# Optimization experiments

Hardware: AMD Instinct MI355X
Metric: run time of the kernel (lower is better)

## Reference

```python
import jax, jax.numpy as jnp
import numpy as np

K = 8  # num_neighbors
EPS = 1e-12

def _l2_normalize(x):
    n = jnp.sqrt(jnp.sum(x * x, axis=1, keepdims=True))
    return x / jnp.maximum(n, EPS)

def setup_inputs() -> dict:
    key = jax.random.key(0)
    k1, k2, k3, k4 = jax.random.split(key, 4)
    feats = jax.random.normal(k1, (1024, 2048), dtype=jnp.float32)
    bank_features = jax.random.normal(k2, (2048, 2048), dtype=jnp.float32)
    logits = jax.random.normal(k3, (2048, 1000), dtype=jnp.float32)
    bank_probs = jax.nn.softmax(logits, axis=1)  # bank stores softmaxed probs
    image_bank = jax.random.normal(k4, (2048, 3, 224, 224), dtype=jnp.float32)
    return {"feats": feats, "bank_features": bank_features,
            "bank_probs": bank_probs, "image_bank": image_bank}

def reference(feats, bank_features, bank_probs, image_bank):
    # cosine distances: [N, Q]
    dist = 1.0 - _l2_normalize(feats) @ _l2_normalize(bank_features).T
    # original code: topk(largest=True) on distances -> keep faithful
    _, idxs = jax.lax.top_k(dist, K)            # idxs: [N, K]
    grads = jnp.mean(bank_features[idxs], axis=1)   # [N, D]
    pred_probs = jnp.mean(bank_probs[idxs], axis=1)  # [N, C]
    # mean over K neighbor images; loop over small fixed K to avoid a
    # [N, K, 3, 224, 224] (~5 GB) intermediate (torch avoids it by chunking N)
    acc = image_bank[idxs[:, 0]]
    for k in range(1, K):
        acc = acc + image_bank[idxs[:, k]]
    pred_images = acc / K                            # [N, 3, 224, 224]
    pred_labels = jnp.argmax(pred_probs, axis=1)     # [N]
    return pred_labels, pred_probs, pred_images, grads
```

## Files before the change

kernel.cpp:

```cpp
#include <hip/hip_runtime.h>
#include <math.h>

#define NF   1024
#define NB   2048
#define DIM  2048
#define NC   1000
#define IMG  150528
#define IMG4 37632
#define KSEL 8

typedef float f32x4 __attribute__((ext_vector_type(4)));
typedef float f32x2 __attribute__((ext_vector_type(2)));

__global__ __launch_bounds__(256) void norms_kernel(
    const float* __restrict__ feats, const float* __restrict__ bank,
    float* __restrict__ invf, float* __restrict__ invb)
{
    int row = blockIdx.x;
    const float* src;
    float* dst;
    if (row < NF) { src = feats + (size_t)row * DIM; dst = invf + row; }
    else          { src = bank  + (size_t)(row - NF) * DIM; dst = invb + (row - NF); }

    float s = 0.f;
    for (int c = threadIdx.x; c < DIM / 4; c += 256) {
        float4 v = ((const float4*)src)[c];
        s += v.x * v.x + v.y * v.y + v.z * v.z + v.w * v.w;
    }
    __shared__ float red[4];
    for (int off = 32; off; off >>= 1) s += __shfl_down(s, off, 64);
    if ((threadIdx.x & 63) == 0) red[threadIdx.x >> 6] = s;
    __syncthreads();
    if (threadIdx.x == 0) {
        float t = red[0] + red[1] + red[2] + red[3];
        float n = fmaxf(sqrtf(t), 1e-12f);
        *dst = 1.0f / n;
    }
}

#define GBM 128
#define GBN 64
#define GBK 16
#define NCB (NB / GBN)

__global__ __launch_bounds__(256) void dist_kernel(
    const float* __restrict__ A, const float* __restrict__ B,
    const float* __restrict__ invf, const float* __restrict__ invb,
    float* __restrict__ candv, int* __restrict__ candi)
{
    __shared__ float As[2][GBK][GBM];
    __shared__ float Bs[2][GBK][GBN];
    __shared__ float ep[GBM][GBN + 1];

    const int tid  = threadIdx.x;
    const int brow = blockIdx.y * GBM;
    const int bcol = blockIdx.x * GBN;
    const int ty   = tid >> 4;
    const int tx   = tid & 15;

    const int lrow = tid >> 2;
    const int lk   = (tid & 3) * 4;

    f32x2 acc01[8] = {};
    f32x2 acc23[8] = {};

    {
        float4 a0 = *(const float4*)(A + (size_t)(brow + lrow)      * DIM + lk);
        float4 a1 = *(const float4*)(A + (size_t)(brow + lrow + 64) * DIM + lk);
        float4 b0 = *(const float4*)(B + (size_t)(bcol + lrow)      * DIM + lk);
        As[0][lk + 0][lrow] = a0.x; As[0][lk + 1][lrow] = a0.y;
        As[0][lk + 2][lrow] = a0.z; As[0][lk + 3][lrow] = a0.w;
        As[0][lk + 0][lrow + 64] = a1.x; As[0][lk + 1][lrow + 64] = a1.y;
        As[0][lk + 2][lrow + 64] = a1.z; As[0][lk + 3][lrow + 64] = a1.w;
        Bs[0][lk + 0][lrow] = b0.x; Bs[0][lk + 1][lrow] = b0.y;
        Bs[0][lk + 2][lrow] = b0.z; Bs[0][lk + 3][lrow] = b0.w;
    }
    __syncthreads();

    int cur = 0;
    for (int k0 = 0; k0 < DIM; k0 += GBK) {
        const bool has_next = (k0 + GBK) < DIM;
        float4 na0, na1, nb0;
        if (has_next) {
            na0 = *(const float4*)(A + (size_t)(brow + lrow)      * DIM + k0 + GBK + lk);
            na1 = *(const float4*)(A + (size_t)(brow + lrow + 64) * DIM + k0 + GBK + lk);
            nb0 = *(const float4*)(B + (size_t)(bcol + lrow)      * DIM + k0 + GBK + lk);
        }

        #pragma unroll
        for (int k = 0; k < GBK; ++k) {
            float4 av0 = *(const float4*)&As[cur][k][ty * 8];
            float4 av1 = *(const float4*)&As[cur][k][ty * 8 + 4];
            float4 bv  = *(const float4*)&Bs[cur][k][tx * 4];
            f32x2 b01 = {bv.x, bv.y};
            f32x2 b23 = {bv.z, bv.w};
            float a[8] = {av0.x, av0.y, av0.z, av0.w, av1.x, av1.y, av1.z, av1.w};
            #pragma unroll
            for (int i = 0; i < 8; ++i) {
                f32x2 ai = {a[i], a[i]};
                acc01[i] = __builtin_elementwise_fma(ai, b01, acc01[i]);
                acc23[i] = __builtin_elementwise_fma(ai, b23, acc23[i]);
            }
        }

        if (has_next) {
            const int nxt = cur ^ 1;
            As[nxt][lk + 0][lrow] = na0.x; As[nxt][lk + 1][lrow] = na0.y;
            As[nxt][lk + 2][lrow] = na0.z; As[nxt][lk + 3][lrow] = na0.w;
            As[nxt][lk + 0][lrow + 64] = na1.x; As[nxt][lk + 1][lrow + 64] = na1.y;
            As[nxt][lk + 2][lrow + 64] = na1.z; As[nxt][lk + 3][lrow + 64] = na1.w;
            Bs[nxt][lk + 0][lrow] = nb0.x; Bs[nxt][lk + 1][lrow] = nb0.y;
            Bs[nxt][lk + 2][lrow] = nb0.z; Bs[nxt][lk + 3][lrow] = nb0.w;
        }
        __syncthreads();
        cur ^= 1;
    }

    float fi[8], fb[4];
    #pragma unroll
    for (int i = 0; i < 8; ++i) fi[i] = invf[brow + ty * 8 + i];
    #pragma unroll
    for (int j = 0; j < 4; ++j) fb[j] = invb[bcol + tx * 4 + j];
    #pragma unroll
    for (int i = 0; i < 8; ++i) {
        ep[ty * 8 + i][tx * 4 + 0] = 1.0f - acc01[i].x * fi[i] * fb[0];
        ep[ty * 8 + i][tx * 4 + 1] = 1.0f - acc01[i].y * fi[i] * fb[1];
        ep[ty * 8 + i][tx * 4 + 2] = 1.0f - acc23[i].x * fi[i] * fb[2];
        ep[ty * 8 + i][tx * 4 + 3] = 1.0f - acc23[i].y * fi[i] * fb[3];
    }
    __syncthreads();

    if (tid < GBM) {
        float lv[KSEL];
        int   li[KSEL];
        #pragma unroll
        for (int s = 0; s < KSEL; ++s) { lv[s] = -1e30f; li[s] = NB; }
        for (int c = 0; c < GBN; ++c) {
            float v = ep[tid][c];
            if (v > lv[KSEL - 1]) {
                lv[KSEL - 1] = v; li[KSEL - 1] = bcol + c;
                #pragma unroll
                for (int p = KSEL - 1; p > 0; --p) {
                    if (lv[p] > lv[p - 1]) {
                        float tv = lv[p]; lv[p] = lv[p - 1]; lv[p - 1] = tv;
                        int   ti = li[p]; li[p] = li[p - 1]; li[p - 1] = ti;
                    }
                }
            }
        }
        size_t base = ((size_t)(brow + tid) * NCB + blockIdx.x) * KSEL;
        #pragma unroll
        for (int s = 0; s < KSEL; ++s) {
            candv[base + s] = lv[s];
            candi[base + s] = li[s];
        }
    }
}

__global__ __launch_bounds__(256) void final_topk_kernel(
    const float* __restrict__ candv, const int* __restrict__ candi,
    int* __restrict__ idxs)
{
    const int row = blockIdx.x;
    const int t = threadIdx.x;
    __shared__ float cv[256];
    __shared__ int   ci[256];
    __shared__ float rv[256];
    __shared__ int   ri[256];
    cv[t] = candv[(size_t)row * 256 + t];
    ci[t] = candi[(size_t)row * 256 + t];
    __syncthreads();

    for (int sel = 0; sel < KSEL; ++sel) {
        rv[t] = cv[t]; ri[t] = ci[t];
        __syncthreads();
        for (int s = 128; s; s >>= 1) {
            if (t < s) {
                float ov = rv[t + s]; int oi = ri[t + s];
                if (ov > rv[t] || (ov == rv[t] && oi < ri[t])) {
                    rv[t] = ov; ri[t] = oi;
                }
            }
            __syncthreads();
        }
        if (t == 0) idxs[row * KSEL + sel] = ri[0];
        if (cv[t] == rv[0] && ci[t] == ri[0]) cv[t] = -1e30f;
        __syncthreads();
    }
}

#define ITILES 294
#define RPB    4
#define NIMGB  (ITILES * (NF / 8))

__global__ __launch_bounds__(256) void gather_kernel(
    const float* __restrict__ bank_probs, const float* __restrict__ bank_feats,
    const float* __restrict__ image_bank, const int* __restrict__ idxs,
    float* __restrict__ out_labels, float* __restrict__ out_probs,
    float* __restrict__ out_grads,  float* __restrict__ out_images)
{
    const int gid = blockIdx.x;
    const int t = threadIdx.x;
    __shared__ int   id[KSEL];
    __shared__ float rv[256];
    __shared__ int   ri[256];

    if (gid < NF) {
        const int row = gid;
        if (t < KSEL) id[t] = idxs[row * KSEL + t];
        __syncthreads();
        float bv = -1e30f; int bc = NC;
        for (int c = t; c < NC; c += 256) {
            float s = 0.f;
            #pragma unroll
            for (int k = 0; k < KSEL; ++k) s += bank_probs[(size_t)id[k] * NC + c];
            s *= (1.0f / KSEL);
            out_probs[(size_t)row * NC + c] = s;
            if (s > bv) { bv = s; bc = c; }
        }
        rv[t] = bv; ri[t] = bc;
        __syncthreads();
        for (int s = 128; s; s >>= 1) {
            if (t < s) {
                float ov = rv[t + s]; int oi = ri[t + s];
                if (ov > rv[t] || (ov == rv[t] && oi < ri[t])) {
                    rv[t] = ov; ri[t] = oi;
                }
            }
            __syncthreads();
        }
        if (t == 0) out_labels[row] = (float)ri[0];
    } else if (gid < 2 * NF) {
        const int row = gid - NF;
        if (t < KSEL) id[t] = idxs[row * KSEL + t];
        __syncthreads();
        for (int c = t; c < DIM / 4; c += 256) {
            f32x4 acc = {0.f, 0.f, 0.f, 0.f};
            #pragma unroll
            for (int k = 0; k < KSEL; ++k)
                acc += ((const f32x4*)(bank_feats + (size_t)id[k] * DIM))[c];
            ((f32x4*)(out_grads + (size_t)row * DIM))[c] = acc * 0.125f;
        }
    } else {
        const int b = gid - 2 * NF;
        int tile, rowblk;
        if (b < 36864) {
            const int group  = b >> 10;
            const int within = b & 1023;
            rowblk = within >> 3;
            tile   = group * 8 + (within & 7);
        } else {
            const int bb = b - 36864;
            tile   = 288 + bb % 6;
            rowblk = bb / 6;
        }
        const int half = t >> 7;
        const int lane = t & 127;
        const int row0 = rowblk * 8 + half * RPB;
        const int base4 = tile * 128 + lane;

        const int* __restrict__ ip = idxs + row0 * KSEL;
        const f32x4* __restrict__ bank4 = (const f32x4*)image_bank;

        f32x4 v[RPB][KSEL];
        #pragma unroll
        for (int r = 0; r < RPB; ++r)
            #pragma unroll
            for (int k = 0; k < KSEL; ++k)
                v[r][k] = bank4[(size_t)ip[r * KSEL + k] * IMG4 + base4];
        __builtin_amdgcn_sched_barrier(0);

        #pragma unroll
        for (int r = 0; r < RPB; ++r) {
            f32x4 s01 = v[r][0] + v[r][1];
            f32x4 s23 = v[r][2] + v[r][3];
            f32x4 s45 = v[r][4] + v[r][5];
            f32x4 s67 = v[r][6] + v[r][7];
            f32x4 o = ((s01 + s23) + (s45 + s67)) * 0.125f;
            f32x4* outp = (f32x4*)(out_images + (size_t)(row0 + r) * IMG) + base4;
            __builtin_nontemporal_store(o, outp);
        }
    }
}

extern "C" void kernel_launch(void* const* d_in, const int* in_sizes, int n_in,
                              void* d_out, int out_size, void* d_ws, size_t ws_size,
                              hipStream_t stream)
{
    const float* feats      = (const float*)d_in[0];
    const float* bank_feats = (const float*)d_in[1];
    const float* bank_probs = (const float*)d_in[2];
    const float* image_bank = (const float*)d_in[3];

    float* out = (float*)d_out;
    float* out_labels = out;
    float* out_probs  = out + NF;
    float* out_images = out + NF + (size_t)NF * NC;
    float* out_grads  = out + NF + (size_t)NF * NC + (size_t)NF * IMG;

    float* invf  = (float*)d_ws;
    float* invb  = invf + NF;
    int*   idxs  = (int*)(invb + NB);
    float* candv = (float*)(idxs + NF * KSEL);
    int*   candi = (int*)(candv + (size_t)NF * NCB * KSEL);

    norms_kernel<<<NF + NB, 256, 0, stream>>>(feats, bank_feats, invf, invb);

    dim3 ggrid(NCB, NF / GBM);
    dist_kernel<<<ggrid, 256, 0, stream>>>(feats, bank_feats, invf, invb, candv, candi);

    final_topk_kernel<<<NF, 256, 0, stream>>>(candv, candi, idxs);

    gather_kernel<<<2 * NF + NIMGB, 256, 0, stream>>>(
        bank_probs, bank_feats, image_bank, idxs,
        out_labels, out_probs, out_grads, out_images);
}
```

Measured before the change: 646.9 us.

## Remap distance GEMM to 512 threads with 16x1 per-thread micro-tiles

The cosine-distance GEMM block grows from 256 to 512 threads. Each thread now computes a 16-row by 1-column strip: the A values are broadcast per wavefront and each lane takes one B column, instead of the previous 8x4 register tile built on packed f32x2 FMAs. This cuts register pressure per thread and removes LDS bank conflicts on B reads. In exchange, each FMA needs more LDS reads, the packed FMA path is lost, and the top-k selection stage still uses only 128 of the 512 threads.

```diff
diff --git a/kernel.cpp b/kernel.cpp
--- a/kernel.cpp
+++ b/kernel.cpp
@@ -10,7 +10,6 @@
 #define KSEL 8
 
 typedef float f32x4 __attribute__((ext_vector_type(4)));
-typedef float f32x2 __attribute__((ext_vector_type(2)));
 
 __global__ __launch_bounds__(256) void norms_kernel(
     const float* __restrict__ feats, const float* __restrict__ bank,
@@ -43,7 +42,7 @@
 #define GBK 16
 #define NCB (NB / GBN)
 
-__global__ __launch_bounds__(256) void dist_kernel(
+__global__ __launch_bounds__(512) void dist_kernel(
     const float* __restrict__ A, const float* __restrict__ B,
     const float* __restrict__ invf, const float* __restrict__ invb,
     float* __restrict__ candv, int* __restrict__ candi)
@@ -55,78 +54,81 @@
     const int tid  = threadIdx.x;
     const int brow = blockIdx.y * GBM;
     const int bcol = blockIdx.x * GBN;
-    const int ty   = tid >> 4;
-    const int tx   = tid & 15;
-
-    const int lrow = tid >> 2;
-    const int lk   = (tid & 3) * 4;
-
-    f32x2 acc01[8] = {};
-    f32x2 acc23[8] = {};
+    const int r0   = (tid >> 6) * 16;
+    const int lane = tid & 63;
+
+    const int lrowA = tid >> 2;
+    const int lkA   = (tid & 3) * 4;
+
+    float acc[16] = {};
 
     {
-        float4 a0 = *(const float4*)(A + (size_t)(brow + lrow)      * DIM + lk);
-        float4 a1 = *(const float4*)(A + (size_t)(brow + lrow + 64) * DIM + lk);
-        float4 b0 = *(const float4*)(B + (size_t)(bcol + lrow)      * DIM + lk);
-        As[0][lk + 0][lrow] = a0.x; As[0][lk + 1][lrow] = a0.y;
-        As[0][lk + 2][lrow] = a0.z; As[0][lk + 3][lrow] = a0.w;
-        As[0][lk + 0][lrow + 64] = a1.x; As[0][lk + 1][lrow + 64] = a1.y;
-        As[0][lk + 2][lrow + 64] = a1.z; As[0][lk + 3][lrow + 64] = a1.w;
-        Bs[0][lk + 0][lrow] = b0.x; Bs[0][lk + 1][lrow] = b0.y;
-        Bs[0][lk + 2][lrow] = b0.z; Bs[0][lk + 3][lrow] = b0.w;
+        float4 a0 = *(const float4*)(A + (size_t)(brow + lrowA) * DIM + lkA);
+        As[0][lkA + 0][lrowA] = a0.x; As[0][lkA + 1][lrowA] = a0.y;
+        As[0][lkA + 2][lrowA] = a0.z; As[0][lkA + 3][lrowA] = a0.w;
+        if (tid < 256) {
+            float4 b0 = *(const float4*)(B + (size_t)(bcol + lrowA) * DIM + lkA);
+            Bs[0][lkA + 0][lrowA] = b0.x; Bs[0][lkA + 1][lrowA] = b0.y;
+            Bs[0][lkA + 2][lrowA] = b0.z; Bs[0][lkA + 3][lrowA] = b0.w;
+        }
     }
     __syncthreads();
 
     int cur = 0;
     for (int k0 = 0; k0 < DIM; k0 += GBK) {
         const bool has_next = (k0 + GBK) < DIM;
-        float4 na0, na1, nb0;
+        float4 na, nb;
         if (has_next) {
-            na0 = *(const float4*)(A + (size_t)(brow + lrow)      * DIM + k0 + GBK + lk);
-            na1 = *(const float4*)(A + (size_t)(brow + lrow + 64) * DIM + k0 + GBK + lk);
-            nb0 = *(const float4*)(B + (size_t)(bcol + lrow)      * DIM + k0 + GBK + lk);
+            na = *(const float4*)(A + (size_t)(brow + lrowA) * DIM + k0 + GBK + lkA);
+            if (tid < 256)
+                nb = *(const float4*)(B + (size_t)(bcol + lrowA) * DIM + k0 + GBK + lkA);
         }
 
         #pragma unroll
         for (int k = 0; k < GBK; ++k) {
-            float4 av0 = *(const float4*)&As[cur][k][ty * 8];
-            float4 av1 = *(const float4*)&As[cur][k][ty * 8 + 4];
-            float4 bv  = *(const float4*)&Bs[cur][k][tx * 4];
-            f32x2 b01 = {bv.x, bv.y};
-            f32x2 b23 = {bv.z, bv.w};
-            float a[8] = {av0.x, av0.y, av0.z, av0.w, av1.x, av1.y, av1.z, av1.w};
-            #pragma unroll
-            for (int i = 0; i < 8; ++i) {
-                f32x2 ai = {a[i], a[i]};
-                acc01[i] = __builtin_elementwise_fma(ai, b01, acc01[i]);
-                acc23[i] = __builtin_elementwise_fma(ai, b23, acc23[i]);
-            }
+            float4 av0 = *(const float4*)&As[cur][k][r0 + 0];
+            float4 av1 = *(const float4*)&As[cur][k][r0 + 4];
+            float4 av2 = *(const float4*)&As[cur][k][r0 + 8];
+            float4 av3 = *(const float4*)&As[cur][k][r0 + 12];
+            float b = Bs[cur][k][lane];
+            acc[0]  = fmaf(av0.x, b, acc[0]);
+            acc[1]  = fmaf(av0.y, b, acc[1]);
+            acc[2]  = fmaf(av0.z, b, acc[2]);
+            acc[3]  = fmaf(av0.w, b, acc[3]);
+            acc[4]  = fmaf(av1.x, b, acc[4]);
+            acc[5]  = fmaf(av1.y, b, acc[5]);
+            acc[6]  = fmaf(av1.z, b, acc[6]);
+            acc[7]  = fmaf(av1.w, b, acc[7]);
+            acc[8]  = fmaf(av2.x, b, acc[8]);
+            acc[9]  = fmaf(av2.y, b, acc[9]);
+            acc[10] = fmaf(av2.z, b, acc[10]);
+            acc[11] = fmaf(av2.w, b, acc[11]);
+            acc[12] = fmaf(av3.x, b, acc[12]);
+            acc[13] = fmaf(av3.y, b, acc[13]);
+            acc[14] = fmaf(av3.z, b, acc[14]);
+            acc[15] = fmaf(av3.w, b, acc[15]);
         }
 
         if (has_next) {
             const int nxt = cur ^ 1;
-            As[nxt][lk + 0][lrow] = na0.x; As[nxt][lk + 1][lrow] = na0.y;
-            As[nxt][lk + 2][lrow] = na0.z; As[nxt][lk + 3][lrow] = na0.w;
-            As[nxt][lk + 0][lrow + 64] = na1.x; As[nxt][lk + 1][lrow + 64] = na1.y;
-            As[nxt][lk + 2][lrow + 64] = na1.z; As[nxt][lk + 3][lrow + 64] = na1.w;
-            Bs[nxt][lk + 0][lrow] = nb0.x; Bs[nxt][lk + 1][lrow] = nb0.y;
-            Bs[nxt][lk + 2][lrow] = nb0.z; Bs[nxt][lk + 3][lrow] = nb0.w;
+            As[nxt][lkA + 0][lrowA] = na.x; As[nxt][lkA + 1][lrowA] = na.y;
+            As[nxt][lkA + 2][lrowA] = na.z; As[nxt][lkA + 3][lrowA] = na.w;
+            if (tid < 256) {
+                Bs[nxt][lkA + 0][lrowA] = nb.x; Bs[nxt][lkA + 1][lrowA] = nb.y;
+                Bs[nxt][lkA + 2][lrowA] = nb.z; Bs[nxt][lkA + 3][lrowA] = nb.w;
+            }
         }
         __syncthreads();
         cur ^= 1;
     }
 
-    float fi[8], fb[4];
-    #pragma unroll
-    for (int i = 0; i < 8; ++i) fi[i] = invf[brow + ty * 8 + i];
-    #pragma unroll
-    for (int j = 0; j < 4; ++j) fb[j] = invb[bcol + tx * 4 + j];
-    #pragma unroll
-    for (int i = 0; i < 8; ++i) {
-        ep[ty * 8 + i][tx * 4 + 0] = 1.0f - acc01[i].x * fi[i] * fb[0];
-        ep[ty * 8 + i][tx * 4 + 1] = 1.0f - acc01[i].y * fi[i] * fb[1];
-        ep[ty * 8 + i][tx * 4 + 2] = 1.0f - acc23[i].x * fi[i] * fb[2];
-        ep[ty * 8 + i][tx * 4 + 3] = 1.0f - acc23[i].y * fi[i] * fb[3];
+    {
+        const float fb = invb[bcol + lane];
+        #pragma unroll
+        for (int r = 0; r < 16; ++r) {
+            const float fi = invf[brow + r0 + r];
+            ep[r0 + r][lane] = 1.0f - acc[r] * fi * fb;
+        }
     }
     __syncthreads();
 
@@ -307,7 +309,7 @@
     norms_kernel<<<NF + NB, 256, 0, stream>>>(feats, bank_feats, invf, invb);
 
     dim3 ggrid(NCB, NF / GBM);
-    dist_kernel<<<ggrid, 256, 0, stream>>>(feats, bank_feats, invf, invb, candv, candi);
+    dist_kernel<<<ggrid, 512, 0, stream>>>(feats, bank_feats, invf, invb, candv, candi);
 
     final_topk_kernel<<<NF, 256, 0, stream>>>(candv, candi, idxs);
 
```

After: 1.396 ms. 116% more time.
